# Optimization experiments

Measured on AMD Instinct MI355X. Metric: run time of the kernel, lower is better.

## Reference

```python
import jax, jax.numpy as jnp
import numpy as np
from jax import lax

K = 1.0        # Lorentz curvature k (manifold = Lorentz(k=1.0))
EPS = 1e-5     # batchnorm eps


def _project(space):
    # Lorentz orthogonal projection from space components: time = sqrt(k + ||space||^2)
    t = jnp.sqrt(jnp.clip(K + jnp.sum(space * space, axis=1, keepdims=True), 1e-8))
    return jnp.concatenate([t, space], axis=1)


def _lconv(x, w, b, stride, pad):
    # LorentzConv2d: conv over all channels (incl. time) -> space channels, then reproject time
    s = lax.conv_general_dilated(x, w, (stride, stride), [(pad, pad), (pad, pad)],
                                 dimension_numbers=('NCHW', 'OIHW', 'NCHW'))
    s = s + b[None, :, None, None]
    return _project(s)


def _lbn(x, gamma, beta):
    # LorentzBatchNorm2d: standard BN (batch stats) on space channels, then reproject time
    s = x[:, 1:]
    mu = jnp.mean(s, axis=(0, 2, 3), keepdims=True)
    var = jnp.var(s, axis=(0, 2, 3), keepdims=True)
    sh = (s - mu) * lax.rsqrt(var + EPS)
    return _project(gamma[None, :, None, None] * sh + beta[None, :, None, None])


def _lrelu(x):
    # manifold relu: relu on space components, reproject time (manifold_dim=1)
    return _project(jax.nn.relu(x[:, 1:]))


def setup_inputs() -> dict:
    key = jax.random.key(0)
    ks = jax.random.split(key, 8)
    B, Cin, Cout, H, W = 16, 32, 64, 128, 128
    so, si = Cout - 1, Cin  # conv produces space channels only

    def kaiming(k, shape):
        fan_in = int(np.prod(shape[1:]))
        return jax.random.normal(k, shape, jnp.float32) * np.sqrt(2.0 / fan_in)

    # input: valid Lorentz points (time recomputed from random space part)
    x = _project(jax.random.normal(ks[0], (B, Cin - 1, H, W), jnp.float32))

    return {
        'x': x,
        'w1': kaiming(ks[1], (so, Cin, 3, 3)),  'b1': jnp.zeros((so,), jnp.float32),
        'g1': jnp.ones((so,), jnp.float32),     'bt1': jnp.zeros((so,), jnp.float32),
        'w2': kaiming(ks[2], (so, Cout, 3, 3)), 'b2': jnp.zeros((so,), jnp.float32),
        'g2': jnp.ones((so,), jnp.float32),     'bt2': jnp.zeros((so,), jnp.float32),
        'wp': kaiming(ks[3], (so, Cin, 1, 1)),  'bp': jnp.zeros((so,), jnp.float32),
        'gp': jnp.ones((so,), jnp.float32),     'btp': jnp.zeros((so,), jnp.float32),
    }


def reference(x, w1, b1, g1, bt1, w2, b2, g2, bt2, wp, bp, gp, btp):
    x2 = _lconv(x, w1, b1, stride=1, pad=1)
    x2 = _lbn(x2, g1, bt1)
    x2 = _lrelu(x2)
    x2 = _lconv(x2, w2, b2, stride=1, pad=1)
    x2 = _lbn(x2, g2, bt2)
    xp = _lconv(x, wp, bp, stride=1, pad=0)  # projection shortcut (input_dim != output_dim)
    xp = _lbn(xp, gp, btp)
    out_space = xp[:, 1:] + x2[:, 1:]
    out = _project(out_space)
    out = _lrelu(out)
    return out
```

## Files before the change

### kernel.cpp

```cpp
#include <hip/hip_runtime.h>
#include <hip/hip_bf16.h>

#define H_ 128
#define W_ 128
#define HW_ 16384
#define B_ 16

using short8 = __attribute__((ext_vector_type(8))) short;
using f32x4  = __attribute__((ext_vector_type(4))) float;

__device__ __forceinline__ unsigned short f2b(float v) {
    __hip_bfloat16 h = __float2bfloat16(v);
    return *reinterpret_cast<unsigned short*>(&h);
}
__device__ __forceinline__ float b2f(unsigned short u) {
    __hip_bfloat16 h = *reinterpret_cast<__hip_bfloat16*>(&u);
    return __bfloat162float(h);
}

__global__ __launch_bounds__(256) void to_nhwc(
    const float* __restrict__ x, unsigned short* __restrict__ xc)
{
    int p = blockIdx.x * 256 + threadIdx.x;
    int b = p >> 14, rem = p & 16383;
    const float* src = x + (size_t)b * 32 * HW_ + rem;
    unsigned short ob[32];
    #pragma unroll
    for (int c = 0; c < 32; ++c) ob[c] = f2b(src[(size_t)c * HW_]);
    unsigned short* dst = xc + (size_t)p * 32;
    #pragma unroll
    for (int k = 0; k < 4; ++k)
        *reinterpret_cast<short8*>(dst + k * 8) = *reinterpret_cast<short8*>(&ob[k * 8]);
}

__global__ __launch_bounds__(256) void prep_w(
    const float* __restrict__ w, unsigned short* __restrict__ wt, int CIN, int KS)
{
    int NCB = CIN >> 5;
    int total = KS * KS * NCB * 4 * 64 * 8;
    for (int i = blockIdx.x * 256 + threadIdx.x; i < total; i += gridDim.x * 256) {
        int j  = i & 7;
        int co = (i >> 3) & 63;
        int kb = (i >> 9) & 3;
        int cb = (i >> 11) % NCB;
        int tap = (i >> 11) / NCB;
        int ky = tap / KS, kx = tap % KS;
        int ci = cb * 32 + kb * 8 + j;
        float v = (co < 63) ? w[((co * CIN + ci) * KS + ky) * KS + kx] : 0.f;
        wt[i] = f2b(v);
    }
}

template<int CIN, int KS, int PAD>
__global__ __launch_bounds__(256) void conv_mfma(
    const unsigned short* __restrict__ in,
    const unsigned short* __restrict__ wt,
    unsigned short* __restrict__ outp,
    float* __restrict__ sums)
{
    constexpr int NCB   = CIN / 32;
    constexpr int XCOLS = W_ + 2 * PAD;
    constexpr int TAPS  = KS * KS;
    constexpr int NK    = TAPS * NCB;
    constexpr int C8    = CIN / 8;
    constexpr int CPP   = C8 + 1;
    constexpr int ROWCH = W_ * C8;
    constexpr int NRC   = ROWCH / 256;
    constexpr int NPRO  = 2 + PAD;

    __shared__ short8 xs[4 * XCOLS * CPP];
    __shared__ short8 wl[NK * 256];

    const int bid = blockIdx.x;
    const int b  = bid >> 4;
    const int y0 = (bid & 15) * 8;
    const int t  = threadIdx.x;
    const int lane = t & 63;
    const int wv = t >> 6;
    const int xbase = wv * 32;
    const int l15 = lane & 15;
    const int q = lane >> 4;

    const short8* in8 = reinterpret_cast<const short8*>(in);
    const short8* wt8 = reinterpret_cast<const short8*>(wt);

    short8 rW[NK];
    #pragma unroll
    for (int j = 0; j < NK; ++j) rW[j] = wt8[j * 256 + t];
    short8 rP[NPRO][NRC];
    #pragma unroll
    for (int rr = 0; rr < NPRO; ++rr) {
        const int yy = y0 - PAD + rr;
        #pragma unroll
        for (int i = 0; i < NRC; ++i) {
            short8 v = {};
            if (yy >= 0 && yy < H_) v = in8[(size_t)(b * H_ + yy) * ROWCH + i * 256 + t];
            rP[rr][i] = v;
        }
    }
    #pragma unroll
    for (int j = 0; j < NK; ++j) wl[j * 256 + t] = rW[j];
    #pragma unroll
    for (int rr = 0; rr < NPRO; ++rr) {
        const int s = ((y0 - PAD + rr) + 4) & 3;
        #pragma unroll
        for (int i = 0; i < NRC; ++i) {
            const int k = i * 256 + t;
            xs[(s * XCOLS + k / C8 + PAD) * CPP + k % C8] = rP[rr][i];
        }
    }
    if constexpr (PAD) {
        short8 z = {};
        for (int i = t; i < 4 * 2 * C8; i += 256) {
            const int s = i / (2 * C8), rest = i % (2 * C8);
            const int pos = (rest / C8) ? (XCOLS - 1) : 0;
            xs[(s * XCOLS + pos) * CPP + rest % C8] = z;
        }
    }
    __syncthreads();

    float sacc[4] = {0.f, 0.f, 0.f, 0.f}, qacc[4] = {0.f, 0.f, 0.f, 0.f};

    for (int y = y0; y < y0 + 8; ++y) {
        short8 rA[NRC];
        const int yp = y + 2;
        #pragma unroll
        for (int i = 0; i < NRC; ++i) {
            short8 v = {};
            if (yp < H_) v = in8[(size_t)(b * H_ + yp) * ROWCH + i * 256 + t];
            rA[i] = v;
        }

        f32x4 acc[2][4];
        #pragma unroll
        for (int f = 0; f < 2; ++f)
            #pragma unroll
            for (int cf = 0; cf < 4; ++cf)
                #pragma unroll
                for (int r = 0; r < 4; ++r) acc[f][cf][r] = 0.f;

        #pragma unroll
        for (int tap = 0; tap < TAPS; ++tap) {
            const int ky = tap / KS, kx = tap % KS;
            const int sb = (((y + ky - PAD) + 4) & 3) * XCOLS;
            #pragma unroll
            for (int cb = 0; cb < NCB; ++cb) {
                const int tc = tap * NCB + cb;
                short8 bf[4];
                #pragma unroll
                for (int cf = 0; cf < 4; ++cf)
                    bf[cf] = wl[(tc * 4 + q) * 64 + cf * 16 + l15];
                short8 af[2];
                #pragma unroll
                for (int f = 0; f < 2; ++f) {
                    const int pos = xbase + f * 16 + l15 + kx;
                    af[f] = xs[(sb + pos) * CPP + cb * 4 + q];
                }
                #pragma unroll
                for (int f = 0; f < 2; ++f)
                    #pragma unroll
                    for (int cf = 0; cf < 4; ++cf)
                        acc[f][cf] = __builtin_amdgcn_mfma_f32_16x16x32_bf16(
                            af[f], bf[cf], acc[f][cf], 0, 0, 0);
            }
        }

        const size_t obase = ((size_t)(b * H_ + y) * W_) * 64;
        #pragma unroll
        for (int f = 0; f < 2; ++f)
            #pragma unroll
            for (int cf = 0; cf < 4; ++cf)
                #pragma unroll
                for (int r = 0; r < 4; ++r) {
                    float v = acc[f][cf][r];
                    int x = xbase + f * 16 + q * 4 + r;
                    int co = cf * 16 + l15;
                    outp[obase + (size_t)x * 64 + co] = f2b(v);
                    sacc[cf] += v;
                    qacc[cf] = fmaf(v, v, qacc[cf]);
                }

        {
            const int s = (y + 2) & 3;
            #pragma unroll
            for (int i = 0; i < NRC; ++i) {
                const int k = i * 256 + t;
                xs[(s * XCOLS + k / C8 + PAD) * CPP + k % C8] = rA[i];
            }
        }
        __syncthreads();
    }

    #pragma unroll
    for (int cf = 0; cf < 4; ++cf) {
        float s = sacc[cf], qq = qacc[cf];
        s += __shfl_xor(s, 16); qq += __shfl_xor(qq, 16);
        s += __shfl_xor(s, 32); qq += __shfl_xor(qq, 32);
        if (q == 0) {
            int co = cf * 16 + l15;
            atomicAdd(&sums[co], s);
            atomicAdd(&sums[64 + co], qq);
        }
    }
}

__global__ void finalize_stats(const float* __restrict__ sums, float* __restrict__ murs)
{
    int set = blockIdx.x, c = threadIdx.x;
    const float invN = 1.f / (16.f * 16384.f);
    float s = sums[set * 128 + c];
    float qv = sums[set * 128 + 64 + c];
    float mu = s * invN;
    float var = qv * invN - mu * mu;
    murs[set * 128 + c] = mu;
    murs[set * 128 + 64 + c] = rsqrtf(fmaxf(var, 0.f) + 1e-5f);
}

__global__ __launch_bounds__(256) void epi1(
    const unsigned short* __restrict__ s1, const float* __restrict__ murs,
    const float* __restrict__ g, const float* __restrict__ bt,
    unsigned short* __restrict__ h)
{
    int p = blockIdx.x * 256 + threadIdx.x;
    const unsigned short* sp = s1 + (size_t)p * 64;
    unsigned short ib[64], ob[64];
    #pragma unroll
    for (int k = 0; k < 8; ++k)
        *reinterpret_cast<short8*>(&ib[k * 8]) = *reinterpret_cast<const short8*>(sp + k * 8);
    float ssq = 0.f;
    #pragma unroll
    for (int c = 0; c < 63; ++c) {
        float v = b2f(ib[c]);
        v = g[c] * ((v - murs[c]) * murs[64 + c]) + bt[c];
        v = fmaxf(v, 0.f);
        ssq = fmaf(v, v, ssq);
        ob[c + 1] = f2b(v);
    }
    ob[0] = f2b(sqrtf(1.f + ssq));
    unsigned short* hp = h + (size_t)p * 64;
    #pragma unroll
    for (int k = 0; k < 8; ++k)
        *reinterpret_cast<short8*>(hp + k * 8) = *reinterpret_cast<short8*>(&ob[k * 8]);
}

__global__ __launch_bounds__(256) void epi2(
    const unsigned short* __restrict__ s2, const unsigned short* __restrict__ spb,
    const float* __restrict__ murs2, const float* __restrict__ mursp,
    const float* __restrict__ g2, const float* __restrict__ bt2,
    const float* __restrict__ gp, const float* __restrict__ btp,
    float* __restrict__ out)
{
    int p = blockIdx.x * 256 + threadIdx.x;
    int b = p >> 14, rem = p & 16383;
    unsigned short i2[64], ip[64];
    #pragma unroll
    for (int k = 0; k < 8; ++k) {
        *reinterpret_cast<short8*>(&i2[k * 8]) =
            *reinterpret_cast<const short8*>(s2 + (size_t)p * 64 + k * 8);
        *reinterpret_cast<short8*>(&ip[k * 8]) =
            *reinterpret_cast<const short8*>(spb + (size_t)p * 64 + k * 8);
    }
    float* ob = out + (size_t)b * 64 * HW_ + rem;
    float ssq = 0.f;
    #pragma unroll
    for (int c = 0; c < 63; ++c) {
        float v2 = b2f(i2[c]);
        v2 = g2[c] * ((v2 - murs2[c]) * murs2[64 + c]) + bt2[c];
        float vp = b2f(ip[c]);
        vp = gp[c] * ((vp - mursp[c]) * mursp[64 + c]) + btp[c];
        float r = fmaxf(v2 + vp, 0.f);
        ssq = fmaf(r, r, ssq);
        ob[(size_t)(c + 1) * HW_] = r;
    }
    ob[0] = sqrtf(1.f + ssq);
}

extern "C" void kernel_launch(void* const* d_in, const int* in_sizes, int n_in,
                              void* d_out, int out_size, void* d_ws, size_t ws_size,
                              hipStream_t stream)
{
    (void)in_sizes; (void)n_in; (void)out_size; (void)ws_size;
    const float* x   = (const float*)d_in[0];
    const float* w1  = (const float*)d_in[1];
    const float* g1  = (const float*)d_in[3];
    const float* bt1 = (const float*)d_in[4];
    const float* w2  = (const float*)d_in[5];
    const float* g2  = (const float*)d_in[7];
    const float* bt2 = (const float*)d_in[8];
    const float* wp  = (const float*)d_in[9];
    const float* gp  = (const float*)d_in[11];
    const float* btp = (const float*)d_in[12];
    float* out = (float*)d_out;
    char* ws = (char*)d_ws;

    unsigned short* xc  = (unsigned short*)(ws);
    unsigned short* s1  = (unsigned short*)(ws + 16777216);
    unsigned short* h   = (unsigned short*)(ws + 50331648);
    unsigned short* s2  = (unsigned short*)(ws + 83886080);
    unsigned short* w1t = (unsigned short*)(ws + 117440512);
    unsigned short* w2t = (unsigned short*)(ws + 117477376);
    unsigned short* wpt = (unsigned short*)(ws + 117551104);
    float* sums = (float*)(ws + 117555200);
    float* murs = (float*)(ws + 117556736);

    hipMemsetAsync(sums, 0, 1536, stream);
    to_nhwc<<<1024, 256, 0, stream>>>(x, xc);
    prep_w<<<72, 256, 0, stream>>>(w1, w1t, 32, 3);
    prep_w<<<144, 256, 0, stream>>>(w2, w2t, 64, 3);
    prep_w<<<8, 256, 0, stream>>>(wp, wpt, 32, 1);

    conv_mfma<32, 3, 1><<<256, 256, 0, stream>>>(xc, w1t, s1, sums);
    finalize_stats<<<1, 64, 0, stream>>>(sums, murs);
    epi1<<<1024, 256, 0, stream>>>(s1, murs, g1, bt1, h);
    conv_mfma<64, 3, 1><<<256, 256, 0, stream>>>(h, w2t, s2, sums + 128);
    conv_mfma<32, 1, 0><<<256, 256, 0, stream>>>(xc, wpt, s1, sums + 256);
    finalize_stats<<<2, 64, 0, stream>>>(sums + 128, murs + 128);
    epi2<<<1024, 256, 0, stream>>>(s2, s1, murs + 128, murs + 256,
                                   g2, bt2, gp, btp, out);
}
```

Before: 302.0 us.

## Use 512-thread conv blocks computing two output rows per iteration

The MFMA conv kernel now runs 8 waves per block instead of 4. Each wave handles a 64-pixel by 32-channel tile (4x2 fragments) of one of two output rows processed together per loop step, and prefetches two input rows into the 4-slot ring buffer. This halves the number of loop iterations and barriers per row and raises wave count per CU to better hide latency. The cost is an extra barrier before the ring-buffer refill, higher register pressure, and a sliding window that must now hold enough rows for two outputs at once.

```diff
diff --git a/kernel.cpp b/kernel.cpp
--- a/kernel.cpp
+++ b/kernel.cpp
@@ -52,7 +52,7 @@
 }
 
 template<int CIN, int KS, int PAD>
-__global__ __launch_bounds__(256) void conv_mfma(
+__global__ __launch_bounds__(512) void conv_mfma(
     const unsigned short* __restrict__ in,
     const unsigned short* __restrict__ wt,
     unsigned short* __restrict__ outp,
@@ -65,11 +65,12 @@
     constexpr int C8    = CIN / 8;
     constexpr int CPP   = C8 + 1;
     constexpr int ROWCH = W_ * C8;
-    constexpr int NRC   = ROWCH / 256;
-    constexpr int NPRO  = 2 + PAD;
+    constexpr int NRC   = ROWCH / 512;
+    constexpr int NPRO  = 2 + 2 * PAD;
+    constexpr int WCH   = NK * 256;
 
     __shared__ short8 xs[4 * XCOLS * CPP];
-    __shared__ short8 wl[NK * 256];
+    __shared__ short8 wl[WCH];
 
     const int bid = blockIdx.x;
     const int b  = bid >> 4;
@@ -77,16 +78,23 @@
     const int t  = threadIdx.x;
     const int lane = t & 63;
     const int wv = t >> 6;
-    const int xbase = wv * 32;
+    const int rsub = wv >> 2;
+    const int xbase = ((wv >> 1) & 1) * 64;
+    const int cobase = (wv & 1) * 32;
     const int l15 = lane & 15;
     const int q = lane >> 4;
 
     const short8* in8 = reinterpret_cast<const short8*>(in);
     const short8* wt8 = reinterpret_cast<const short8*>(wt);
 
-    short8 rW[NK];
-    #pragma unroll
-    for (int j = 0; j < NK; ++j) rW[j] = wt8[j * 256 + t];
+    constexpr int NW = (WCH + 511) / 512;
+    short8 rW[NW];
+    #pragma unroll
+    for (int j0 = 0; j0 < WCH; j0 += 512) {
+        short8 v = {};
+        if (j0 + t < WCH) v = wt8[j0 + t];
+        rW[j0 / 512] = v;
+    }
     short8 rP[NPRO][NRC];
     #pragma unroll
     for (int rr = 0; rr < NPRO; ++rr) {
@@ -94,24 +102,25 @@
         #pragma unroll
         for (int i = 0; i < NRC; ++i) {
             short8 v = {};
-            if (yy >= 0 && yy < H_) v = in8[(size_t)(b * H_ + yy) * ROWCH + i * 256 + t];
+            if (yy >= 0 && yy < H_) v = in8[(size_t)(b * H_ + yy) * ROWCH + i * 512 + t];
             rP[rr][i] = v;
         }
     }
     #pragma unroll
-    for (int j = 0; j < NK; ++j) wl[j * 256 + t] = rW[j];
+    for (int j0 = 0; j0 < WCH; j0 += 512)
+        if (j0 + t < WCH) wl[j0 + t] = rW[j0 / 512];
     #pragma unroll
     for (int rr = 0; rr < NPRO; ++rr) {
         const int s = ((y0 - PAD + rr) + 4) & 3;
         #pragma unroll
         for (int i = 0; i < NRC; ++i) {
-            const int k = i * 256 + t;
+            const int k = i * 512 + t;
             xs[(s * XCOLS + k / C8 + PAD) * CPP + k % C8] = rP[rr][i];
         }
     }
     if constexpr (PAD) {
         short8 z = {};
-        for (int i = t; i < 4 * 2 * C8; i += 256) {
+        for (int i = t; i < 4 * 2 * C8; i += 512) {
             const int s = i / (2 * C8), rest = i % (2 * C8);
             const int pos = (rest / C8) ? (XCOLS - 1) : 0;
             xs[(s * XCOLS + pos) * CPP + rest % C8] = z;
@@ -119,85 +128,92 @@
     }
     __syncthreads();
 
-    float sacc[4] = {0.f, 0.f, 0.f, 0.f}, qacc[4] = {0.f, 0.f, 0.f, 0.f};
-
-    for (int y = y0; y < y0 + 8; ++y) {
-        short8 rA[NRC];
-        const int yp = y + 2;
-        #pragma unroll
-        for (int i = 0; i < NRC; ++i) {
-            short8 v = {};
-            if (yp < H_) v = in8[(size_t)(b * H_ + yp) * ROWCH + i * 256 + t];
-            rA[i] = v;
-        }
-
-        f32x4 acc[2][4];
-        #pragma unroll
-        for (int f = 0; f < 2; ++f)
-            #pragma unroll
-            for (int cf = 0; cf < 4; ++cf)
+    float sacc[2] = {0.f, 0.f}, qacc[2] = {0.f, 0.f};
+
+    for (int y = y0; y < y0 + 8; y += 2) {
+        short8 rA[2][NRC];
+        #pragma unroll
+        for (int rr = 0; rr < 2; ++rr) {
+            const int yp = y + 2 + PAD + rr;
+            #pragma unroll
+            for (int i = 0; i < NRC; ++i) {
+                short8 v = {};
+                if (yp < H_) v = in8[(size_t)(b * H_ + yp) * ROWCH + i * 512 + t];
+                rA[rr][i] = v;
+            }
+        }
+
+        const int yr = y + rsub;
+        f32x4 acc[4][2];
+        #pragma unroll
+        for (int f = 0; f < 4; ++f)
+            #pragma unroll
+            for (int cf = 0; cf < 2; ++cf)
                 #pragma unroll
                 for (int r = 0; r < 4; ++r) acc[f][cf][r] = 0.f;
 
         #pragma unroll
         for (int tap = 0; tap < TAPS; ++tap) {
             const int ky = tap / KS, kx = tap % KS;
-            const int sb = (((y + ky - PAD) + 4) & 3) * XCOLS;
+            const int sb = (((yr + ky - PAD) + 4) & 3) * XCOLS;
             #pragma unroll
             for (int cb = 0; cb < NCB; ++cb) {
                 const int tc = tap * NCB + cb;
-                short8 bf[4];
-                #pragma unroll
-                for (int cf = 0; cf < 4; ++cf)
-                    bf[cf] = wl[(tc * 4 + q) * 64 + cf * 16 + l15];
-                short8 af[2];
-                #pragma unroll
-                for (int f = 0; f < 2; ++f) {
+                short8 bf[2];
+                #pragma unroll
+                for (int cf = 0; cf < 2; ++cf)
+                    bf[cf] = wl[(tc * 4 + q) * 64 + cobase + cf * 16 + l15];
+                short8 af[4];
+                #pragma unroll
+                for (int f = 0; f < 4; ++f) {
                     const int pos = xbase + f * 16 + l15 + kx;
                     af[f] = xs[(sb + pos) * CPP + cb * 4 + q];
                 }
                 #pragma unroll
-                for (int f = 0; f < 2; ++f)
+                for (int f = 0; f < 4; ++f)
                     #pragma unroll
-                    for (int cf = 0; cf < 4; ++cf)
+                    for (int cf = 0; cf < 2; ++cf)
                         acc[f][cf] = __builtin_amdgcn_mfma_f32_16x16x32_bf16(
                             af[f], bf[cf], acc[f][cf], 0, 0, 0);
             }
         }
 
-        const size_t obase = ((size_t)(b * H_ + y) * W_) * 64;
-        #pragma unroll
-        for (int f = 0; f < 2; ++f)
-            #pragma unroll
-            for (int cf = 0; cf < 4; ++cf)
+        const size_t obase = ((size_t)(b * H_ + yr) * W_) * 64;
+        #pragma unroll
+        for (int f = 0; f < 4; ++f)
+            #pragma unroll
+            for (int cf = 0; cf < 2; ++cf)
                 #pragma unroll
                 for (int r = 0; r < 4; ++r) {
                     float v = acc[f][cf][r];
                     int x = xbase + f * 16 + q * 4 + r;
-                    int co = cf * 16 + l15;
+                    int co = cobase + cf * 16 + l15;
                     outp[obase + (size_t)x * 64 + co] = f2b(v);
                     sacc[cf] += v;
                     qacc[cf] = fmaf(v, v, qacc[cf]);
                 }
 
-        {
-            const int s = (y + 2) & 3;
+        __syncthreads();
+
+        #pragma unroll
+        for (int rr = 0; rr < 2; ++rr) {
+            const int s = (y + 2 + PAD + rr) & 3;
             #pragma unroll
             for (int i = 0; i < NRC; ++i) {
-                const int k = i * 256 + t;
-                xs[(s * XCOLS + k / C8 + PAD) * CPP + k % C8] = rA[i];
+                const int k = i * 512 + t;
+                xs[(s * XCOLS + k / C8 + PAD) * CPP + k % C8] = rA[rr][i];
             }
         }
         __syncthreads();
     }
 
     #pragma unroll
-    for (int cf = 0; cf < 4; ++cf) {
+    for (int cf = 0; cf < 2; ++cf) {
         float s = sacc[cf], qq = qacc[cf];
         s += __shfl_xor(s, 16); qq += __shfl_xor(qq, 16);
         s += __shfl_xor(s, 32); qq += __shfl_xor(qq, 32);
         if (q == 0) {
-            int co = cf * 16 + l15;
+            int co = cobase + cf * 16 + l15;
             atomicAdd(&sums[co], s);
             atomicAdd(&sums[64 + co], qq);
         }
@@ -309,11 +325,11 @@
     prep_w<<<144, 256, 0, stream>>>(w2, w2t, 64, 3);
     prep_w<<<8, 256, 0, stream>>>(wp, wpt, 32, 1);
 
-    conv_mfma<32, 3, 1><<<256, 256, 0, stream>>>(xc, w1t, s1, sums);
+    conv_mfma<32, 3, 1><<<256, 512, 0, stream>>>(xc, w1t, s1, sums);
     finalize_stats<<<1, 64, 0, stream>>>(sums, murs);
     epi1<<<1024, 256, 0, stream>>>(s1, murs, g1, bt1, h);
-    conv_mfma<64, 3, 1><<<256, 256, 0, stream>>>(h, w2t, s2, sums + 128);
-    conv_mfma<32, 1, 0><<<256, 256, 0, stream>>>(xc, wpt, s1, sums + 256);
+    conv_mfma<64, 3, 1><<<256, 512, 0, stream>>>(h, w2t, s2, sums + 128);
+    conv_mfma<32, 1, 0><<<256, 512, 0, stream>>>(xc, wpt, s1, sums + 256);
     finalize_stats<<<2, 64, 0, stream>>>(sums + 128, murs + 128);
     epi2<<<1024, 256, 0, stream>>>(s2, s1, murs + 128, murs + 256,
                                    g2, bt2, gp, btp, out);
```

Result: no change. 296.9 us (-1.7%).
